# Kernel tuning notes

Measured on AMD Instinct MI355X. Metric: run time of the kernel, lower is better.

Reference implementation:

```python
import jax, jax.numpy as jnp
import numpy as np

N_NODES = 100000
N_EDGES = 1600000
N_GRAPHS = 1000
H = 128
F_IN = 128
F_EDGE = 16
DEPTH = 4


def setup_inputs() -> dict:
    key = jax.random.key(0)
    ks = jax.random.split(key, 10)
    s = 1.0 / np.sqrt(H)
    x = jax.random.normal(ks[0], (N_NODES, F_IN), dtype=jnp.float32)
    edge_index = jax.random.randint(ks[1], (2, N_EDGES), 0, N_NODES, dtype=jnp.int32)
    edge_attr = jax.random.normal(ks[2], (N_EDGES, F_EDGE), dtype=jnp.float32)
    batch = jnp.sort(jax.random.randint(ks[3], (N_NODES,), 0, N_GRAPHS, dtype=jnp.int32))
    W0 = jax.random.normal(ks[4], (F_IN, H), dtype=jnp.float32) * s
    b0 = jnp.zeros((H,), dtype=jnp.float32)
    W1 = jax.random.normal(ks[5], (DEPTH, H, H), dtype=jnp.float32) * s
    b1 = jnp.zeros((DEPTH, H), dtype=jnp.float32)
    W2 = jax.random.normal(ks[6], (DEPTH, H, H), dtype=jnp.float32) * s
    b2 = jnp.zeros((DEPTH, H), dtype=jnp.float32)
    Wf = jax.random.normal(ks[7], (H, 1), dtype=jnp.float32) * s
    bf = jnp.zeros((1,), dtype=jnp.float32)
    return {"x": x, "edge_index": edge_index, "edge_attr": edge_attr, "batch": batch,
            "W0": W0, "b0": b0, "W1": W1, "b1": b1, "W2": W2, "b2": b2, "Wf": Wf, "bf": bf}


def reference(x, edge_index, edge_attr, batch, W0, b0, W1, b1, W2, b2, Wf, bf):
    # edge_attr is read by the original forward but never used in the math.
    src, dst = edge_index[0], edge_index[1]
    n = x.shape[0]
    h0 = jax.nn.relu(x @ W0 + b0)  # [N, H]
    h = h0
    for i in range(DEPTH):
        # GINConv (eps=0): MLP(x + sum_{j in N(i)} x_j); messages flow src -> dst
        agg = jax.ops.segment_sum(h[src], dst, num_segments=n)  # [N, H]
        z = h + agg
        z = jax.nn.relu(z @ W1[i] + b1[i]) @ W2[i] + b2[i]
        # residual then relu (dropout p=0.02 is identity at eval)
        h = jax.nn.relu(z + h0)
    pooled = jax.ops.segment_sum(h, batch, num_segments=N_GRAPHS)  # [G, H]
    out = (pooled @ Wf + bf)[:, 0]  # [G]
    return out
```

## Files before the change

### kernel.cpp

```cpp
#include <hip/hip_runtime.h>

#define N_NODES 100000
#define N_EDGES 1600000
#define N_GRAPHS 1000
#define H 128
#define DEPTH 4
#define NB 391
#define BCAP 4864

typedef __attribute__((ext_vector_type(8))) short bf16x8;
typedef __attribute__((ext_vector_type(4))) float f32x4;

__device__ __forceinline__ unsigned short f2bf(float f) {
  unsigned int u = __float_as_uint(f);
  u += 0x7FFF + ((u >> 16) & 1);
  return (unsigned short)(u >> 16);
}
__device__ __forceinline__ float bflo(unsigned int v) { return __uint_as_float(v << 16); }
__device__ __forceinline__ float bfhi(unsigned int v) { return __uint_as_float(v & 0xFFFF0000u); }

__global__ __launch_bounds__(256) void k_bcnt(const int* __restrict__ dst, int* __restrict__ gcnt) {
  __shared__ int c[NB];
  int tid = threadIdx.x, e0 = blockIdx.x * 4096;
  for (int i = tid; i < NB; i += 256) c[i] = 0;
  __syncthreads();
#pragma unroll
  for (int i = 0; i < 16; ++i) {
    int e = e0 + i * 256 + tid;
    if (e < N_EDGES) atomicAdd(&c[dst[e] >> 8], 1);
  }
  __syncthreads();
  for (int i = tid; i < NB; i += 256)
    if (c[i]) atomicAdd(&gcnt[i], c[i]);
}

__global__ __launch_bounds__(512) void k_bscan(const int* __restrict__ gcnt, int* __restrict__ boff,
                                               int* __restrict__ cursor) {
  __shared__ int sh[512];
  int t = threadIdx.x;
  int v = (t < NB) ? gcnt[t] : 0;
  sh[t] = v;
  __syncthreads();
  for (int s = 1; s < 512; s <<= 1) {
    int x = (t >= s) ? sh[t - s] : 0;
    __syncthreads();
    sh[t] += x;
    __syncthreads();
  }
  if (t < NB) {
    int e = sh[t] - v;
    boff[t] = e;
    cursor[t] = e;
  }
  if (t == 0) boff[NB] = N_EDGES;
}

__global__ __launch_bounds__(256) void k_bucket(const int* __restrict__ src, const int* __restrict__ dst,
                                                int* __restrict__ cursor, unsigned int* __restrict__ ebuf) {
  __shared__ int cnt[NB];
  __shared__ int base[NB];
  int tid = threadIdx.x;
  int e0 = blockIdx.x * 4096;
  for (int i = tid; i < NB; i += 256) cnt[i] = 0;
  __syncthreads();
  unsigned int pk[16];
  int bk[16], rk[16];
#pragma unroll
  for (int i = 0; i < 16; ++i) {
    int e = e0 + i * 256 + tid;
    if (e < N_EDGES) {
      int s = src[e], d = dst[e];
      bk[i] = d >> 8;
      pk[i] = ((unsigned int)(d & 255) << 17) | (unsigned int)s;
      rk[i] = atomicAdd(&cnt[bk[i]], 1);
    } else
      bk[i] = -1;
  }
  __syncthreads();
  for (int i = tid; i < NB; i += 256)
    base[i] = cnt[i] ? atomicAdd(&cursor[i], cnt[i]) : 0;
  __syncthreads();
#pragma unroll
  for (int i = 0; i < 16; ++i)
    if (bk[i] >= 0) ebuf[base[bk[i]] + rk[i]] = pk[i];
}

__global__ __launch_bounds__(256) void k_bsort(const unsigned int* __restrict__ ebuf,
                                               const int* __restrict__ boff,
                                               int* __restrict__ csr, int* __restrict__ offs) {
  __shared__ unsigned int arr[BCAP];
  __shared__ unsigned int srt[BCAP];
  __shared__ unsigned short rnk[BCAP];
  __shared__ int cnt[256];
  __shared__ int off[257];
  int b = blockIdx.x, tid = threadIdx.x;
  int beg = boff[b], end = boff[b + 1];
  int ce = min(end - beg, BCAP);
  cnt[tid] = 0;
  __syncthreads();
  for (int i = tid; i < ce; i += 256) {
    unsigned int p = ebuf[beg + i];
    arr[i] = p;
    rnk[i] = (unsigned short)atomicAdd(&cnt[p >> 17], 1);
  }
  __syncthreads();
  int v = cnt[tid];
  off[tid + 1] = v;
  if (tid == 0) off[0] = 0;
  __syncthreads();
  for (int s = 1; s < 256; s <<= 1) {
    int x = (tid + 1 > s) ? off[tid + 1 - s] : 0;
    __syncthreads();
    off[tid + 1] += x;
    __syncthreads();
  }
  for (int i = tid; i < ce; i += 256) {
    unsigned int p = arr[i];
    srt[off[p >> 17] + rnk[i]] = p & 0x1FFFF;
  }
  __syncthreads();
  for (int i = tid; i < ce; i += 256) csr[beg + i] = (int)srt[i];
  int node = (b << 8) + tid;
  if (node < N_NODES) offs[node] = beg + off[tid];
  if (b == NB - 1 && tid == 0) offs[N_NODES] = N_EDGES;
}

__device__ __forceinline__ void stage_w(const float* __restrict__ Wg, unsigned short* Wt, int tid) {
  for (int idx = tid; idx < 2048; idx += 256) {
    int ng4 = idx & 31, kp = idx >> 5;
    float4 r0 = *(const float4*)&Wg[(2 * kp) * H + 4 * ng4];
    float4 r1 = *(const float4*)&Wg[(2 * kp + 1) * H + 4 * ng4];
    unsigned int p0 = (unsigned int)f2bf(r0.x) | ((unsigned int)f2bf(r1.x) << 16);
    unsigned int p1 = (unsigned int)f2bf(r0.y) | ((unsigned int)f2bf(r1.y) << 16);
    unsigned int p2 = (unsigned int)f2bf(r0.z) | ((unsigned int)f2bf(r1.z) << 16);
    unsigned int p3 = (unsigned int)f2bf(r0.w) | ((unsigned int)f2bf(r1.w) << 16);
    *(unsigned int*)&Wt[(4 * ng4 + 0) * 136 + 2 * kp] = p0;
    *(unsigned int*)&Wt[(4 * ng4 + 1) * 136 + 2 * kp] = p1;
    *(unsigned int*)&Wt[(4 * ng4 + 2) * 136 + 2 * kp] = p2;
    *(unsigned int*)&Wt[(4 * ng4 + 3) * 136 + 2 * kp] = p3;
  }
}

__global__ __launch_bounds__(256) void k_lin(const float* __restrict__ in, const float* __restrict__ Wg,
                                             const float* __restrict__ bg, unsigned short* __restrict__ outp) {
  __shared__ unsigned short Wt[128 * 136];
  __shared__ unsigned short zs[64 * 136];
  int tid = threadIdx.x;
  int lane = tid & 63, w = tid >> 6;
  int q = lane >> 4, l16 = lane & 15;
  int n0 = blockIdx.x * 64;

  stage_w(Wg, Wt, tid);

  int row = n0 + w * 16 + l16;
  int rr = (row < N_NODES) ? row : 0;
  bf16x8 afrag[4];
#pragma unroll
  for (int ks = 0; ks < 4; ++ks) {
    const float* p = &in[(size_t)rr * H + ks * 32 + q * 8];
    float4 f0 = *(const float4*)p;
    float4 f1 = *(const float4*)(p + 4);
    bf16x8 a;
    a[0] = (short)f2bf(f0.x); a[1] = (short)f2bf(f0.y); a[2] = (short)f2bf(f0.z); a[3] = (short)f2bf(f0.w);
    a[4] = (short)f2bf(f1.x); a[5] = (short)f2bf(f1.y); a[6] = (short)f2bf(f1.z); a[7] = (short)f2bf(f1.w);
    afrag[ks] = a;
  }
  f32x4 acc[8];
#pragma unroll
  for (int ct = 0; ct < 8; ++ct) acc[ct] = (f32x4){0.f, 0.f, 0.f, 0.f};
  __syncthreads();
#pragma unroll
  for (int ct = 0; ct < 8; ++ct)
#pragma unroll
    for (int ks = 0; ks < 4; ++ks) {
      bf16x8 b = *(bf16x8*)&Wt[(ct * 16 + l16) * 136 + ks * 32 + q * 8];
      acc[ct] = __builtin_amdgcn_mfma_f32_16x16x32_bf16(afrag[ks], b, acc[ct], 0, 0, 0);
    }
#pragma unroll
  for (int ct = 0; ct < 8; ++ct) {
    float bb = bg[ct * 16 + l16];
#pragma unroll
    for (int r = 0; r < 4; ++r) {
      float v = fmaxf(acc[ct][r] + bb, 0.f);
      zs[(w * 16 + q * 4 + r) * 136 + ct * 16 + l16] = f2bf(v);
    }
  }
  __syncthreads();
  int node = tid >> 2, cb = (tid & 3) * 32;
  if (n0 + node < N_NODES) {
#pragma unroll
    for (int i = 0; i < 4; ++i) {
      uint4 v = *(uint4*)&zs[node * 136 + cb + i * 8];
      *(uint4*)&outp[(size_t)(n0 + node) * H + cb + i * 8] = v;
    }
  }
}

__global__ __launch_bounds__(256) void k_agg(const unsigned short* __restrict__ hin, const int* __restrict__ offs,
                                             const int* __restrict__ csr, unsigned short* __restrict__ zin) {
  int node = blockIdx.x * 8 + (threadIdx.x >> 5);
  int l = threadIdx.x & 31;
  if (node >= N_NODES) return;
  const uint2* hu = (const uint2*)hin;
  uint2 self = hu[(size_t)node * 32 + l];
  float a0 = bflo(self.x), a1 = bfhi(self.x), a2 = bflo(self.y), a3 = bfhi(self.y);
  int beg = offs[node], end = offs[node + 1];
  for (int e = beg; e < end; e += 32) {
    int cnt = min(32, end - e);
    int idx = (l < cnt) ? csr[e + l] : 0;
    int j = 0;
    for (; j + 8 <= cnt; j += 8) {
      int s0 = __shfl(idx, j, 32), s1 = __shfl(idx, j + 1, 32);
      int s2 = __shfl(idx, j + 2, 32), s3 = __shfl(idx, j + 3, 32);
      int s4 = __shfl(idx, j + 4, 32), s5 = __shfl(idx, j + 5, 32);
      int s6 = __shfl(idx, j + 6, 32), s7 = __shfl(idx, j + 7, 32);
      uint2 v0 = hu[(size_t)s0 * 32 + l];
      uint2 v1 = hu[(size_t)s1 * 32 + l];
      uint2 v2 = hu[(size_t)s2 * 32 + l];
      uint2 v3 = hu[(size_t)s3 * 32 + l];
      uint2 v4 = hu[(size_t)s4 * 32 + l];
      uint2 v5 = hu[(size_t)s5 * 32 + l];
      uint2 v6 = hu[(size_t)s6 * 32 + l];
      uint2 v7 = hu[(size_t)s7 * 32 + l];
      a0 += bflo(v0.x); a1 += bfhi(v0.x); a2 += bflo(v0.y); a3 += bfhi(v0.y);
      a0 += bflo(v1.x); a1 += bfhi(v1.x); a2 += bflo(v1.y); a3 += bfhi(v1.y);
      a0 += bflo(v2.x); a1 += bfhi(v2.x); a2 += bflo(v2.y); a3 += bfhi(v2.y);
      a0 += bflo(v3.x); a1 += bfhi(v3.x); a2 += bflo(v3.y); a3 += bfhi(v3.y);
      a0 += bflo(v4.x); a1 += bfhi(v4.x); a2 += bflo(v4.y); a3 += bfhi(v4.y);
      a0 += bflo(v5.x); a1 += bfhi(v5.x); a2 += bflo(v5.y); a3 += bfhi(v5.y);
      a0 += bflo(v6.x); a1 += bfhi(v6.x); a2 += bflo(v6.y); a3 += bfhi(v6.y);
      a0 += bflo(v7.x); a1 += bfhi(v7.x); a2 += bflo(v7.y); a3 += bfhi(v7.y);
    }
    for (; j + 4 <= cnt; j += 4) {
      int s0 = __shfl(idx, j, 32), s1 = __shfl(idx, j + 1, 32);
      int s2 = __shfl(idx, j + 2, 32), s3 = __shfl(idx, j + 3, 32);
      uint2 v0 = hu[(size_t)s0 * 32 + l];
      uint2 v1 = hu[(size_t)s1 * 32 + l];
      uint2 v2 = hu[(size_t)s2 * 32 + l];
      uint2 v3 = hu[(size_t)s3 * 32 + l];
      a0 += bflo(v0.x); a1 += bfhi(v0.x); a2 += bflo(v0.y); a3 += bfhi(v0.y);
      a0 += bflo(v1.x); a1 += bfhi(v1.x); a2 += bflo(v1.y); a3 += bfhi(v1.y);
      a0 += bflo(v2.x); a1 += bfhi(v2.x); a2 += bflo(v2.y); a3 += bfhi(v2.y);
      a0 += bflo(v3.x); a1 += bfhi(v3.x); a2 += bflo(v3.y); a3 += bfhi(v3.y);
    }
    for (; j < cnt; ++j) {
      int s = __shfl(idx, j, 32);
      uint2 v = hu[(size_t)s * 32 + l];
      a0 += bflo(v.x); a1 += bfhi(v.x); a2 += bflo(v.y); a3 += bfhi(v.y);
    }
  }
  unsigned long long o = (unsigned long long)((unsigned int)f2bf(a0) | ((unsigned int)f2bf(a1) << 16)) |
                         ((unsigned long long)((unsigned int)f2bf(a2) | ((unsigned int)f2bf(a3) << 16)) << 32);
  __builtin_nontemporal_store(o, (unsigned long long*)zin + (size_t)node * 32 + l);
}

__global__ __launch_bounds__(256) void k_mlp(const unsigned short* __restrict__ zin,
                                             const float* __restrict__ W1g, const float* __restrict__ b1g,
                                             const float* __restrict__ W2g, const float* __restrict__ b2g,
                                             const unsigned short* __restrict__ h0, unsigned short* __restrict__ h) {
  __shared__ unsigned short Wt[128 * 136];
  __shared__ unsigned short zs[64 * 136];
  int tid = threadIdx.x;
  int lane = tid & 63, w = tid >> 6;
  int q = lane >> 4, l16 = lane & 15;
  int n0 = blockIdx.x * 64;

  stage_w(W1g, Wt, tid);

  int row = n0 + w * 16 + l16;
  int rr = (row < N_NODES) ? row : 0;
  bf16x8 afrag[4];
#pragma unroll
  for (int ks = 0; ks < 4; ++ks)
    afrag[ks] = *(bf16x8*)&zin[(size_t)rr * H + ks * 32 + q * 8];

  f32x4 acc[8];
#pragma unroll
  for (int ct = 0; ct < 8; ++ct) acc[ct] = (f32x4){0.f, 0.f, 0.f, 0.f};
  __syncthreads();
#pragma unroll
  for (int ct = 0; ct < 8; ++ct)
#pragma unroll
    for (int ks = 0; ks < 4; ++ks) {
      bf16x8 b = *(bf16x8*)&Wt[(ct * 16 + l16) * 136 + ks * 32 + q * 8];
      acc[ct] = __builtin_amdgcn_mfma_f32_16x16x32_bf16(afrag[ks], b, acc[ct], 0, 0, 0);
    }
  __syncthreads();
  stage_w(W2g, Wt, tid);
#pragma unroll
  for (int ct = 0; ct < 8; ++ct) {
    float bb = b1g[ct * 16 + l16];
#pragma unroll
    for (int r = 0; r < 4; ++r) {
      float v = fmaxf(acc[ct][r] + bb, 0.f);
      zs[(w * 16 + q * 4 + r) * 136 + ct * 16 + l16] = f2bf(v);
    }
  }
  __syncthreads();
  bf16x8 a2[4];
#pragma unroll
  for (int ks = 0; ks < 4; ++ks)
    a2[ks] = *(bf16x8*)&zs[(w * 16 + l16) * 136 + ks * 32 + q * 8];
  f32x4 acc2[8];
#pragma unroll
  for (int ct = 0; ct < 8; ++ct) acc2[ct] = (f32x4){0.f, 0.f, 0.f, 0.f};
#pragma unroll
  for (int ct = 0; ct < 8; ++ct)
#pragma unroll
    for (int ks = 0; ks < 4; ++ks) {
      bf16x8 b = *(bf16x8*)&Wt[(ct * 16 + l16) * 136 + ks * 32 + q * 8];
      acc2[ct] = __builtin_amdgcn_mfma_f32_16x16x32_bf16(a2[ks], b, acc2[ct], 0, 0, 0);
    }
#pragma unroll
  for (int ct = 0; ct < 8; ++ct) {
    float bb = b2g[ct * 16 + l16];
#pragma unroll
    for (int r = 0; r < 4; ++r) {
      float v = acc2[ct][r] + bb;
      zs[(w * 16 + q * 4 + r) * 136 + ct * 16 + l16] = f2bf(v);
    }
  }
  __syncthreads();
  int node = tid >> 2, cb = (tid & 3) * 32;
  if (n0 + node < N_NODES) {
    size_t base = (size_t)(n0 + node) * H + cb;
#pragma unroll
    for (int i = 0; i < 4; ++i) {
      uint4 zv = *(uint4*)&zs[node * 136 + cb + i * 8];
      uint4 hv = *(const uint4*)&h0[base + i * 8];
      unsigned int zr[4] = {zv.x, zv.y, zv.z, zv.w};
      unsigned int hr[4] = {hv.x, hv.y, hv.z, hv.w};
      uint4 o;
      unsigned int orr[4];
#pragma unroll
      for (int j = 0; j < 4; ++j) {
        float a = fmaxf(bflo(zr[j]) + bflo(hr[j]), 0.f);
        float b = fmaxf(bfhi(zr[j]) + bfhi(hr[j]), 0.f);
        orr[j] = (unsigned int)f2bf(a) | ((unsigned int)f2bf(b) << 16);
      }
      o.x = orr[0]; o.y = orr[1]; o.z = orr[2]; o.w = orr[3];
      *(uint4*)&h[base + i * 8] = o;
    }
  }
}

__global__ void k_starts(const int* __restrict__ batch, int* __restrict__ starts) {
  int n = blockIdx.x * 256 + threadIdx.x;
  if (n >= N_NODES) return;
  int b = batch[n];
  if (n == 0) {
    for (int g = 0; g <= b; ++g) starts[g] = 0;
  } else {
    int bp = batch[n - 1];
    for (int g = bp + 1; g <= b; ++g) starts[g] = n;
  }
  if (n == N_NODES - 1) {
    for (int g = b + 1; g <= N_GRAPHS; ++g) starts[g] = N_NODES;
  }
}

__global__ __launch_bounds__(256) void k_pool(const unsigned short* __restrict__ h, const int* __restrict__ starts,
                                              const float* __restrict__ Wf, const float* __restrict__ bf_,
                                              float* __restrict__ out) {
  __shared__ float r[4];
  int g = blockIdx.x, tid = threadIdx.x;
  int lane = tid & 63, w = tid >> 6;
  int beg = starts[g], end = starts[g + 1];
  const unsigned int* hu = (const unsigned int*)h;
  float sx = 0.f, sy = 0.f;
  for (int n = beg + w; n < end; n += 4) {
    unsigned int v = hu[(size_t)n * 64 + lane];
    sx += bflo(v);
    sy += bfhi(v);
  }
  float val = sx * Wf[2 * lane] + sy * Wf[2 * lane + 1];
#pragma unroll
  for (int off = 32; off > 0; off >>= 1) val += __shfl_down(val, off);
  if (lane == 0) r[w] = val;
  __syncthreads();
  if (tid == 0) out[g] = r[0] + r[1] + r[2] + r[3] + bf_[0];
}

extern "C" void kernel_launch(void* const* d_in, const int* in_sizes, int n_in,
                              void* d_out, int out_size, void* d_ws, size_t ws_size,
                              hipStream_t stream) {
  const float* x = (const float*)d_in[0];
  const int* ei = (const int*)d_in[1];
  const int* srcv = ei;
  const int* dstv = ei + N_EDGES;
  const int* batch = (const int*)d_in[3];
  const float* W0 = (const float*)d_in[4];
  const float* b0 = (const float*)d_in[5];
  const float* W1 = (const float*)d_in[6];
  const float* b1 = (const float*)d_in[7];
  const float* W2 = (const float*)d_in[8];
  const float* b2 = (const float*)d_in[9];
  const float* Wf = (const float*)d_in[10];
  const float* bf_ = (const float*)d_in[11];
  float* out = (float*)d_out;

  char* ws = (char*)d_ws;
  size_t o = 0;
  auto alloc = [&](size_t bytes) {
    size_t r = o;
    o = (o + bytes + 255) & ~(size_t)255;
    return r;
  };
  int* offs = (int*)(ws + alloc((N_NODES + 1) * sizeof(int)));
  int* gcnt = (int*)(ws + alloc(NB * sizeof(int)));
  int* boff = (int*)(ws + alloc((NB + 1) * sizeof(int)));
  int* cursor = (int*)(ws + alloc(NB * sizeof(int)));
  unsigned int* ebuf = (unsigned int*)(ws + alloc((size_t)N_EDGES * 4));
  int* csr = (int*)(ws + alloc((size_t)N_EDGES * sizeof(int)));
  int* starts = (int*)(ws + alloc((N_GRAPHS + 1) * sizeof(int)));
  unsigned short* h0 = (unsigned short*)(ws + alloc((size_t)N_NODES * H * 2));
  unsigned short* h = (unsigned short*)(ws + alloc((size_t)N_NODES * H * 2));
  unsigned short* zin = (unsigned short*)(ws + alloc((size_t)N_NODES * H * 2));

  hipMemsetAsync(gcnt, 0, NB * sizeof(int), stream);
  k_bcnt<<<NB, 256, 0, stream>>>(dstv, gcnt);
  k_bscan<<<1, 512, 0, stream>>>(gcnt, boff, cursor);
  k_bucket<<<NB, 256, 0, stream>>>(srcv, dstv, cursor, ebuf);
  k_bsort<<<NB, 256, 0, stream>>>(ebuf, boff, csr, offs);
  k_starts<<<(N_NODES + 255) / 256, 256, 0, stream>>>(batch, starts);

  const int nblk = (N_NODES + 63) / 64;
  k_lin<<<nblk, 256, 0, stream>>>(x, W0, b0, h0);
  for (int i = 0; i < DEPTH; ++i) {
    const unsigned short* hin = (i == 0) ? h0 : h;
    k_agg<<<(N_NODES + 7) / 8, 256, 0, stream>>>(hin, offs, csr, zin);
    k_mlp<<<nblk, 256, 0, stream>>>(zin, W1 + (size_t)i * H * H, b1 + (size_t)i * H,
                                    W2 + (size_t)i * H * H, b2 + (size_t)i * H, h0, h);
  }
  k_pool<<<N_GRAPHS, 256, 0, stream>>>(h, starts, Wf, bf_, out);
}
```

Before: 672.5 us.

## Pre-convert weights to bf16 once and double MLP block tile to 128 nodes

Adds a k_wprep kernel that converts and transposes W0, W1 and W2 into padded bf16 layouts in a workspace buffer once per call. The linear and MLP kernels then stage weights with plain 16-byte copies instead of converting fp32 per block. Blocks grow to 512 threads covering 128 nodes, which halves the number of weight stagings. The cost is an extra small launch, more LDS per block, and possibly lower occupancy.

```diff
diff --git a/kernel.cpp b/kernel.cpp
--- a/kernel.cpp
+++ b/kernel.cpp
@@ -7,6 +7,8 @@
 #define DEPTH 4
 #define NB 391
 #define BCAP 4864
+#define WPITCH 136
+#define WSLOT (H * WPITCH)
 
 typedef __attribute__((ext_vector_type(8))) short bf16x8;
 typedef __attribute__((ext_vector_type(4))) float f32x4;
@@ -125,32 +127,45 @@
   if (b == NB - 1 && tid == 0) offs[N_NODES] = N_EDGES;
 }
 
-__device__ __forceinline__ void stage_w(const float* __restrict__ Wg, unsigned short* Wt, int tid) {
-  for (int idx = tid; idx < 2048; idx += 256) {
-    int ng4 = idx & 31, kp = idx >> 5;
-    float4 r0 = *(const float4*)&Wg[(2 * kp) * H + 4 * ng4];
-    float4 r1 = *(const float4*)&Wg[(2 * kp + 1) * H + 4 * ng4];
-    unsigned int p0 = (unsigned int)f2bf(r0.x) | ((unsigned int)f2bf(r1.x) << 16);
-    unsigned int p1 = (unsigned int)f2bf(r0.y) | ((unsigned int)f2bf(r1.y) << 16);
-    unsigned int p2 = (unsigned int)f2bf(r0.z) | ((unsigned int)f2bf(r1.z) << 16);
-    unsigned int p3 = (unsigned int)f2bf(r0.w) | ((unsigned int)f2bf(r1.w) << 16);
-    *(unsigned int*)&Wt[(4 * ng4 + 0) * 136 + 2 * kp] = p0;
-    *(unsigned int*)&Wt[(4 * ng4 + 1) * 136 + 2 * kp] = p1;
-    *(unsigned int*)&Wt[(4 * ng4 + 2) * 136 + 2 * kp] = p2;
-    *(unsigned int*)&Wt[(4 * ng4 + 3) * 136 + 2 * kp] = p3;
-  }
-}
-
-__global__ __launch_bounds__(256) void k_lin(const float* __restrict__ in, const float* __restrict__ Wg,
+__global__ __launch_bounds__(256) void k_wprep(const float* __restrict__ W0, const float* __restrict__ W1,
+                                               const float* __restrict__ W2, unsigned short* __restrict__ wb) {
+  int m = blockIdx.x >> 3, part = blockIdx.x & 7, tid = threadIdx.x;
+  const float* src = (m == 0) ? W0 : ((m <= DEPTH) ? W1 + (size_t)(m - 1) * H * H : W2 + (size_t)(m - 1 - DEPTH) * H * H);
+  unsigned short* dst = wb + (size_t)m * WSLOT;
+  int idx = part * 256 + tid;
+  int ng4 = idx & 31, kp = idx >> 5;
+  float4 r0 = *(const float4*)&src[(2 * kp) * H + 4 * ng4];
+  float4 r1 = *(const float4*)&src[(2 * kp + 1) * H + 4 * ng4];
+  unsigned int p0 = (unsigned int)f2bf(r0.x) | ((unsigned int)f2bf(r1.x) << 16);
+  unsigned int p1 = (unsigned int)f2bf(r0.y) | ((unsigned int)f2bf(r1.y) << 16);
+  unsigned int p2 = (unsigned int)f2bf(r0.z) | ((unsigned int)f2bf(r1.z) << 16);
+  unsigned int p3 = (unsigned int)f2bf(r0.w) | ((unsigned int)f2bf(r1.w) << 16);
+  *(unsigned int*)&dst[(4 * ng4 + 0) * WPITCH + 2 * kp] = p0;
+  *(unsigned int*)&dst[(4 * ng4 + 1) * WPITCH + 2 * kp] = p1;
+  *(unsigned int*)&dst[(4 * ng4 + 2) * WPITCH + 2 * kp] = p2;
+  *(unsigned int*)&dst[(4 * ng4 + 3) * WPITCH + 2 * kp] = p3;
+}
+
+__device__ __forceinline__ void stage_wb(const unsigned short* __restrict__ Wg, unsigned short* Wt, int tid) {
+#pragma unroll
+  for (int i = 0; i < 4; ++i) {
+    int c = tid + i * 512;
+    *(uint4*)&Wt[c * 8] = *(const uint4*)&Wg[c * 8];
+  }
+  int c = tid + 2048;
+  if (c < 2176) *(uint4*)&Wt[c * 8] = *(const uint4*)&Wg[c * 8];
+}
+
+__global__ __launch_bounds__(512) void k_lin(const float* __restrict__ in, const unsigned short* __restrict__ w0t,
                                              const float* __restrict__ bg, unsigned short* __restrict__ outp) {
-  __shared__ unsigned short Wt[128 * 136];
-  __shared__ unsigned short zs[64 * 136];
+  __shared__ __align__(16) unsigned short Wt[WSLOT];
+  __shared__ __align__(16) unsigned short zs[128 * 136];
   int tid = threadIdx.x;
   int lane = tid & 63, w = tid >> 6;
   int q = lane >> 4, l16 = lane & 15;
-  int n0 = blockIdx.x * 64;
-
-  stage_w(Wg, Wt, tid);
+  int n0 = blockIdx.x * 128;
+
+  stage_wb(w0t, Wt, tid);
 
   int row = n0 + w * 16 + l16;
   int rr = (row < N_NODES) ? row : 0;
@@ -173,7 +188,7 @@
   for (int ct = 0; ct < 8; ++ct)
 #pragma unroll
     for (int ks = 0; ks < 4; ++ks) {
-      bf16x8 b = *(bf16x8*)&Wt[(ct * 16 + l16) * 136 + ks * 32 + q * 8];
+      bf16x8 b = *(bf16x8*)&Wt[(ct * 16 + l16) * WPITCH + ks * 32 + q * 8];
       acc[ct] = __builtin_amdgcn_mfma_f32_16x16x32_bf16(afrag[ks], b, acc[ct], 0, 0, 0);
     }
 #pragma unroll
@@ -254,18 +269,18 @@
   __builtin_nontemporal_store(o, (unsigned long long*)zin + (size_t)node * 32 + l);
 }
 
-__global__ __launch_bounds__(256) void k_mlp(const unsigned short* __restrict__ zin,
-                                             const float* __restrict__ W1g, const float* __restrict__ b1g,
-                                             const float* __restrict__ W2g, const float* __restrict__ b2g,
+__global__ __launch_bounds__(512) void k_mlp(const unsigned short* __restrict__ zin,
+                                             const unsigned short* __restrict__ w1t, const float* __restrict__ b1g,
+                                             const unsigned short* __restrict__ w2t, const float* __restrict__ b2g,
                                              const unsigned short* __restrict__ h0, unsigned short* __restrict__ h) {
-  __shared__ unsigned short Wt[128 * 136];
-  __shared__ unsigned short zs[64 * 136];
+  __shared__ __align__(16) unsigned short Wt[WSLOT];
+  __shared__ __align__(16) unsigned short zs[128 * 136];
   int tid = threadIdx.x;
   int lane = tid & 63, w = tid >> 6;
   int q = lane >> 4, l16 = lane & 15;
-  int n0 = blockIdx.x * 64;
-
-  stage_w(W1g, Wt, tid);
+  int n0 = blockIdx.x * 128;
+
+  stage_wb(w1t, Wt, tid);
 
   int row = n0 + w * 16 + l16;
   int rr = (row < N_NODES) ? row : 0;
@@ -282,11 +297,11 @@
   for (int ct = 0; ct < 8; ++ct)
 #pragma unroll
     for (int ks = 0; ks < 4; ++ks) {
-      bf16x8 b = *(bf16x8*)&Wt[(ct * 16 + l16) * 136 + ks * 32 + q * 8];
+      bf16x8 b = *(bf16x8*)&Wt[(ct * 16 + l16) * WPITCH + ks * 32 + q * 8];
       acc[ct] = __builtin_amdgcn_mfma_f32_16x16x32_bf16(afrag[ks], b, acc[ct], 0, 0, 0);
     }
   __syncthreads();
-  stage_w(W2g, Wt, tid);
+  stage_wb(w2t, Wt, tid);
 #pragma unroll
   for (int ct = 0; ct < 8; ++ct) {
     float bb = b1g[ct * 16 + l16];
@@ -308,7 +323,7 @@
   for (int ct = 0; ct < 8; ++ct)
 #pragma unroll
     for (int ks = 0; ks < 4; ++ks) {
-      bf16x8 b = *(bf16x8*)&Wt[(ct * 16 + l16) * 136 + ks * 32 + q * 8];
+      bf16x8 b = *(bf16x8*)&Wt[(ct * 16 + l16) * WPITCH + ks * 32 + q * 8];
       acc2[ct] = __builtin_amdgcn_mfma_f32_16x16x32_bf16(a2[ks], b, acc2[ct], 0, 0, 0);
     }
 #pragma unroll
@@ -416,21 +431,24 @@
   unsigned short* h0 = (unsigned short*)(ws + alloc((size_t)N_NODES * H * 2));
   unsigned short* h = (unsigned short*)(ws + alloc((size_t)N_NODES * H * 2));
   unsigned short* zin = (unsigned short*)(ws + alloc((size_t)N_NODES * H * 2));
+  unsigned short* wbuf = (unsigned short*)(ws + alloc((size_t)9 * WSLOT * 2));
 
   hipMemsetAsync(gcnt, 0, NB * sizeof(int), stream);
+  k_wprep<<<72, 256, 0, stream>>>(W0, W1, W2, wbuf);
   k_bcnt<<<NB, 256, 0, stream>>>(dstv, gcnt);
   k_bscan<<<1, 512, 0, stream>>>(gcnt, boff, cursor);
   k_bucket<<<NB, 256, 0, stream>>>(srcv, dstv, cursor, ebuf);
   k_bsort<<<NB, 256, 0, stream>>>(ebuf, boff, csr, offs);
   k_starts<<<(N_NODES + 255) / 256, 256, 0, stream>>>(batch, starts);
 
-  const int nblk = (N_NODES + 63) / 64;
-  k_lin<<<nblk, 256, 0, stream>>>(x, W0, b0, h0);
+  const int nblk = (N_NODES + 127) / 128;
+  k_lin<<<nblk, 512, 0, stream>>>(x, wbuf, b0, h0);
   for (int i = 0; i < DEPTH; ++i) {
     const unsigned short* hin = (i == 0) ? h0 : h;
     k_agg<<<(N_NODES + 7) / 8, 256, 0, stream>>>(hin, offs, csr, zin);
-    k_mlp<<<nblk, 256, 0, stream>>>(zin, W1 + (size_t)i * H * H, b1 + (size_t)i * H,
-                                    W2 + (size_t)i * H * H, b2 + (size_t)i * H, h0, h);
+    k_mlp<<<nblk, 512, 0, stream>>>(zin, wbuf + (size_t)(1 + i) * WSLOT, b1 + (size_t)i * H,
+                                    wbuf + (size_t)(1 + DEPTH + i) * WSLOT, b2 + (size_t)i * H,
+                                    h0, h);
   }
   k_pool<<<N_GRAPHS, 256, 0, stream>>>(h, starts, Wf, bf_, out);
 }
```

New measurement: 601.4 us. 10.6% less time.
